# Kernel optimization log

Measured on AMD Instinct MI355X. Metric: run time of the kernel, lower is better.

Reference implementation:

```python
import jax, jax.numpy as jnp
import numpy as np

B, NV, NP, D, K = 8, 2048, 4096, 64, 8  # shapes per batch, vtx/pts counts, feat dim, num_interp
NEG = -1e9


def _unit(x):
    return x / jnp.clip(jnp.linalg.norm(x, axis=-1, keepdims=True), 1e-12)


def _gather(v, idx):
    # v: [B, N, C], idx: [B, Q, K] -> [B, Q, K, C]
    return jax.vmap(lambda a, i: a[i])(v, idx)


def setup_inputs() -> dict:
    key = jax.random.key(0)
    k1, k2, k3, k4, k5 = jax.random.split(key, 5)
    return {
        "vtx": jax.random.normal(k1, (B * NV, 3), jnp.float32),
        "pts": jax.random.normal(k2, (B * NP, 3), jnp.float32),
        "vtx_feature": jax.random.normal(k3, (B * NV, D), jnp.float32),
        "pts_feature": jax.random.normal(k4, (B * NP, D), jnp.float32),
        "vismask_logits": jax.random.normal(k5, (B * NV, 1), jnp.float32),
    }


def reference(vtx, pts, vtx_feature, pts_feature, vismask_logits):
    # --- per-batch min-max normalization of sigmoid(vismask) (serial loop in torch) ---
    vm = jax.nn.sigmoid(vismask_logits).reshape(B, NV, 1)
    vmin = vm.min(axis=1, keepdims=True)
    vmax = vm.max(axis=1, keepdims=True)
    vm = (vm - vmin) / (vmax - vmin)

    vtxb = vtx.reshape(B, NV, 3)
    ptsb = pts.reshape(B, NP, 3)
    vf = vtx_feature.reshape(B, NV, D)
    pf = pts_feature.reshape(B, NP, D)

    # --- cosine KNN: for each vtx, k nearest pts by cosine similarity ---
    sim = jnp.einsum('bnd,bmd->bnm', _unit(vf), _unit(pf))  # [B,NV,NP]
    _, idx = jax.lax.top_k(sim, K)                           # [B,NV,K]

    nbr_pts = _gather(ptsb, idx)                             # [B,NV,K,3]
    nbr_pf = _gather(pf, idx)                                # [B,NV,K,D]
    euclid = nbr_pts - vtxb[:, :, None, :]
    # raw (unnormalized) dot product, weighted by vismask of the query vertex
    fsim = jnp.sum(nbr_pf * vf[:, :, None, :], axis=-1, keepdims=True) * vm[:, :, None, :]
    # scatter_add over assign_index[0] == sum over the K grouped neighbors
    flow_init = jnp.sum(euclid * fsim, axis=2) / jnp.sum(fsim, axis=2)  # [B,NV,3]

    # --- interpolate flow at invisible vertices from visible ones (2nd cosine KNN) ---
    vis = vm >= 0.5                                          # [B,NV,1]
    vfn = _unit(vf)
    sim2 = jnp.einsum('bnd,bmd->bnm', vfn, vfn)              # [B,NV,NV]
    sim2 = jnp.where(vis[:, :, 0][:, None, :], sim2, NEG)    # keys restricted to visible vtx
    _, idx2 = jax.lax.top_k(sim2, K)                         # [B,NV,K]

    nbr_vf = _gather(vf, idx2)                               # [B,NV,K,D]
    nbr_flow = _gather(flow_init, idx2)                      # [B,NV,K,3]
    fsim2 = jnp.sum(nbr_vf * vf[:, :, None, :], axis=-1, keepdims=True)
    invis_flow = jnp.sum(nbr_flow * fsim2, axis=2) / jnp.sum(fsim2, axis=2)

    flow = jnp.where(vis, flow_init, invis_flow)             # flow_init[invis] = invis_flow
    l1_points = jnp.concatenate([flow, vm], axis=-1)         # [B,NV,4]
    return l1_points.reshape(B * NV, 4)
```

## Files before the change

### kernel.cpp

```cpp
#include <hip/hip_runtime.h>
#include <math.h>

#define BB 8
#define NVV 2048
#define NPP 4096
#define DD 64
#define NQ (BB * NVV)
#define QT (NQ / 16)

typedef __attribute__((ext_vector_type(8))) short short8;
typedef __attribute__((ext_vector_type(8))) unsigned short ushort8;
typedef __attribute__((ext_vector_type(4))) float f32x4;

typedef __attribute__((address_space(1))) const unsigned gu32;
typedef __attribute__((address_space(3))) unsigned su32;


__device__ __forceinline__ unsigned short bf16rn(float x) {
  unsigned u = __float_as_uint(x);
  return (unsigned short)((u + 0x7FFFu + ((u >> 16) & 1u)) >> 16);
}
__device__ __forceinline__ float bf2f(unsigned short h) {
  return __uint_as_float(((unsigned)h) << 16);
}

__device__ __forceinline__ void net8(unsigned* a, unsigned v) {
#pragma unroll
  for (int k = 0; k < 7; k++) {
    unsigned r;
    asm("v_med3_u32 %0, %1, %2, %3" : "=v"(r) : "v"(v), "v"(a[k]), "v"(a[k + 1]));
    a[k] = r;
  }
  a[7] = a[7] > v ? a[7] : v;
}

__device__ __forceinline__ unsigned fkey(float s) {
  unsigned u = __float_as_uint(s);
  return ((int)u < 0) ? ~u : (u | 0x80000000u);
}

__global__ __launch_bounds__(256) void k_prep(const float* __restrict__ logits,
                                              const float* __restrict__ vf,
                                              const float* __restrict__ pf,
                                              float* __restrict__ vm,
                                              float* __restrict__ inv_vf_s,
                                              float* __restrict__ inv_pf_s,
                                              unsigned short* __restrict__ vfh,
                                              unsigned short* __restrict__ vfl,
                                              unsigned short* __restrict__ pfh,
                                              unsigned short* __restrict__ pfl,
                                              float* __restrict__ out) {
  int bid = blockIdx.x, t = threadIdx.x;
  if (bid >= 768) {
    int b = bid - 768;
    __shared__ float smn[4], smx[4];
    float vals[8];
    float mn = 1e30f, mx = -1e30f;
#pragma unroll
    for (int i = 0; i < 8; i++) {
      float x = logits[b * NVV + t + i * 256];
      float s = 1.0f / (1.0f + expf(-x));
      vals[i] = s;
      mn = fminf(mn, s);
      mx = fmaxf(mx, s);
    }
    for (int o = 32; o; o >>= 1) {
      mn = fminf(mn, __shfl_xor(mn, o, 64));
      mx = fmaxf(mx, __shfl_xor(mx, o, 64));
    }
    int w = t >> 6;
    if ((t & 63) == 0) { smn[w] = mn; smx[w] = mx; }
    __syncthreads();
    mn = fminf(fminf(smn[0], smn[1]), fminf(smn[2], smn[3]));
    mx = fmaxf(fmaxf(smx[0], smx[1]), fmaxf(smx[2], smx[3]));
    float range = mx - mn;
#pragma unroll
    for (int i = 0; i < 8; i++) {
      float v = (vals[i] - mn) / range;
      int g = b * NVV + t + i * 256;
      vm[g] = v;
      out[g * 4 + 3] = v;
    }
  } else {
    int xcd = bid & 7, kk = bid >> 3;
    int wsel = t >> 6;
    int lane = t & 63, c = lane & 15, quad = (lane >> 4) & 3;
    const float* src;
    unsigned short *dh, *dl;
    float* ginv;
    int tile;
    if (kk < 32) {
      tile = xcd * 128 + kk * 4 + wsel;
      src = vf; dh = vfh; dl = vfl; ginv = inv_vf_s;
    } else {
      tile = xcd * 256 + (kk - 32) * 4 + wsel;
      src = pf; dh = pfh; dl = pfl; ginv = inv_pf_s;
    }
    int row = tile * 16 + c;
    const float* rp = src + (size_t)row * DD + quad * 8;
    float4 a0 = *(const float4*)(rp);
    float4 b0 = *(const float4*)(rp + 4);
    float4 a1 = *(const float4*)(rp + 32);
    float4 b1 = *(const float4*)(rp + 36);
    float xs[16] = {a0.x, a0.y, a0.z, a0.w, b0.x, b0.y, b0.z, b0.w,
                    a1.x, a1.y, a1.z, a1.w, b1.x, b1.y, b1.z, b1.w};
    float ss = 0.f;
#pragma unroll
    for (int j = 0; j < 16; j++) ss = fmaf(xs[j], xs[j], ss);
    ss += __shfl_xor(ss, 16, 64);
    ss += __shfl_xor(ss, 32, 64);
    float inv = 1.0f / fmaxf(sqrtf(ss), 1e-12f);
    if (quad == 0) ginv[row] = 16384.0f * inv;
    ushort8 h, l;
    size_t s0 = (size_t)tile * 128 + lane;
#pragma unroll
    for (int j = 0; j < 8; j++) {
      float xn = xs[j] * inv;
      unsigned short hj = bf16rn(xn);
      h[j] = hj;
      l[j] = bf16rn(xn - bf2f(hj));
    }
    *(ushort8*)(dh + s0 * 8) = h;
    *(ushort8*)(dl + s0 * 8) = l;
#pragma unroll
    for (int j = 0; j < 8; j++) {
      float xn = xs[8 + j] * inv;
      unsigned short hj = bf16rn(xn);
      h[j] = hj;
      l[j] = bf16rn(xn - bf2f(hj));
    }
    *(ushort8*)(dh + (s0 + 64) * 8) = h;
    *(ushort8*)(dl + (s0 + 64) * 8) = l;
  }
}

#define LOADK(d0, d1, d2, d3, KH, KL, tile) do {            \
    size_t bo_ = (size_t)(tile) * 1024 + lane * 8;          \
    d0 = *(const short8*)((KH) + bo_);                      \
    d1 = *(const short8*)((KH) + bo_ + 512);                \
    d2 = *(const short8*)((KL) + bo_);                      \
    d3 = *(const short8*)((KL) + bo_ + 512);                \
  } while (0)

#define MFMA6(c_, h0_, h1_, l0_, l1_) do {                                  \
    c_ = __builtin_amdgcn_mfma_f32_16x16x32_bf16(h0_, qh0, c_, 0, 0, 0);    \
    c_ = __builtin_amdgcn_mfma_f32_16x16x32_bf16(h1_, qh1, c_, 0, 0, 0);    \
    c_ = __builtin_amdgcn_mfma_f32_16x16x32_bf16(h0_, ql0, c_, 0, 0, 0);    \
    c_ = __builtin_amdgcn_mfma_f32_16x16x32_bf16(h1_, ql1, c_, 0, 0, 0);    \
    c_ = __builtin_amdgcn_mfma_f32_16x16x32_bf16(l0_, qh0, c_, 0, 0, 0);    \
    c_ = __builtin_amdgcn_mfma_f32_16x16x32_bf16(l1_, qh1, c_, 0, 0, 0);    \
  } while (0)

#define COMP1(h0_, h1_, l0_, l1_, b16_) do {                                \
    f32x4 c_ = {0.f, 0.f, 0.f, 0.f};                                        \
    MFMA6(c_, h0_, h1_, l0_, l1_);                                          \
    unsigned u0_ = (unsigned)fmaxf(fmaf(c_[0], 520000.0f, 520000.0f), 0.0f);\
    net8(tvA, (u0_ << 12) | (unsigned)((b16_) + 0));                        \
    unsigned u1_ = (unsigned)fmaxf(fmaf(c_[1], 520000.0f, 520000.0f), 0.0f);\
    net8(tvA, (u1_ << 12) | (unsigned)((b16_) + 1));                        \
    unsigned u2_ = (unsigned)fmaxf(fmaf(c_[2], 520000.0f, 520000.0f), 0.0f);\
    net8(tvB, (u2_ << 12) | (unsigned)((b16_) + 2));                        \
    unsigned u3_ = (unsigned)fmaxf(fmaf(c_[3], 520000.0f, 520000.0f), 0.0f);\
    net8(tvB, (u3_ << 12) | (unsigned)((b16_) + 3));                        \
  } while (0)

#define COMP2(h0_, h1_, l0_, l1_, b16_, mp_) do {                           \
    float4 mv_ = *(const float4*)(mp_);                                     \
    f32x4 c_ = {0.f, 0.f, 0.f, 0.f};                                        \
    MFMA6(c_, h0_, h1_, l0_, l1_);                                          \
    unsigned u0_ = (unsigned)fmaxf(fmaf(c_[0], 520000.0f, 520000.0f), 0.0f);\
    unsigned p0_ = (u0_ << 12) | (unsigned)((b16_) + 0);                    \
    net8(tvA, (mv_.x >= 0.5f) ? p0_ : 0u);                                  \
    unsigned u1_ = (unsigned)fmaxf(fmaf(c_[1], 520000.0f, 520000.0f), 0.0f);\
    unsigned p1_ = (u1_ << 12) | (unsigned)((b16_) + 1);                    \
    net8(tvA, (mv_.y >= 0.5f) ? p1_ : 0u);                                  \
    unsigned u2_ = (unsigned)fmaxf(fmaf(c_[2], 520000.0f, 520000.0f), 0.0f);\
    unsigned p2_ = (u2_ << 12) | (unsigned)((b16_) + 2);                    \
    net8(tvB, (mv_.z >= 0.5f) ? p2_ : 0u);                                  \
    unsigned u3_ = (unsigned)fmaxf(fmaf(c_[3], 520000.0f, 520000.0f), 0.0f);\
    unsigned p3_ = (u3_ << 12) | (unsigned)((b16_) + 3);                    \
    net8(tvB, (mv_.w >= 0.5f) ? p3_ : 0u);                                  \
  } while (0)

__global__ __launch_bounds__(256)
void k_knn(const unsigned short* __restrict__ vfh, const unsigned short* __restrict__ vfl,
           const unsigned short* __restrict__ pfh, const unsigned short* __restrict__ pfl,
           const float* __restrict__ vm, unsigned* __restrict__ pc2,
           const float* __restrict__ vf, const float* __restrict__ pf,
           const float* __restrict__ pts, const float* __restrict__ vtx,
           const float* __restrict__ inv_pf_s,
           float* __restrict__ flow_ws, float* __restrict__ out) {
  __shared__ unsigned mg[2][2][16][8];
  __shared__ unsigned cand[16][16];
  __shared__ float rowsLds[4][16][256];
  __shared__ float qrows[16][64];

  int p = blockIdx.x;
  int xcd = p & 7, j = p >> 3;
  int qt_g = xcd * 128 + j;
  int batch = xcd;
  int w = (int)threadIdx.x >> 6;
  int ck = w >> 1, hf = w & 1;
  int lane = threadIdx.x & 63, col = lane & 15, quad = lane >> 4;

  size_t ab = (size_t)qt_g * 1024 + lane * 8;
  short8 qh0 = *(const short8*)(vfh + ab);
  short8 qh1 = *(const short8*)(vfh + ab + 512);
  short8 ql0 = *(const short8*)(vfl + ab);
  short8 ql1 = *(const short8*)(vfl + ab + 512);
  asm volatile("" : "+a"(qh0), "+a"(qh1), "+a"(ql0), "+a"(ql1));

  unsigned tvA[8], tvB[8];

#pragma unroll
  for (int k = 0; k < 8; k++) { tvA[k] = 0u; tvB[k] = 0u; }
  {
    int bt0 = batch * 256 + ck * 128 + hf * 64;
    int tb16 = (ck * 128 + hf * 64) * 16 + quad * 4;
    short8 ah0, ah1, al0, al1, bh0, bh1, bl0, bl1;
    LOADK(ah0, ah1, al0, al1, pfh, pfl, bt0);
#pragma unroll 1
    for (int kt = 0; kt < 62; kt += 2) {
      LOADK(bh0, bh1, bl0, bl1, pfh, pfl, bt0 + kt + 1);
      COMP1(ah0, ah1, al0, al1, tb16 + kt * 16);
      LOADK(ah0, ah1, al0, al1, pfh, pfl, bt0 + kt + 2);
      COMP1(bh0, bh1, bl0, bl1, tb16 + (kt + 1) * 16);
    }
    LOADK(bh0, bh1, bl0, bl1, pfh, pfl, bt0 + 63);
    COMP1(ah0, ah1, al0, al1, tb16 + 62 * 16);
    COMP1(bh0, bh1, bl0, bl1, tb16 + 63 * 16);
  }
#pragma unroll
  for (int k = 0; k < 8; k++) net8(tvA, tvB[k]);
#pragma unroll
  for (int m = 16; m <= 32; m <<= 1) {
    unsigned ov[8];
#pragma unroll
    for (int k = 0; k < 8; k++) ov[k] = (unsigned)__shfl_xor((int)tvA[k], m, 64);
#pragma unroll
    for (int k = 7; k >= 0; k--) net8(tvA, ov[k]);
  }
  if (hf == 1 && quad == 0) {
#pragma unroll
    for (int k = 0; k < 8; k++) mg[0][ck][col][k] = tvA[k];
  }
  __syncthreads();
  if (hf == 0 && quad == 0) {
#pragma unroll
    for (int k = 0; k < 8; k++) net8(tvA, mg[0][ck][col][k]);
#pragma unroll
    for (int k = 0; k < 8; k++)
      cand[col][ck * 8 + k] = tvA[k];
  }
  __syncthreads();

  {
    int tt = (int)threadIdx.x;
    unsigned pkp = cand[tt >> 4][tt & 15];
    const float* gsrc = pf + (size_t)(batch * NPP + (int)(pkp & 0xFFFu)) * DD;
#pragma unroll
    for (int jj = 0; jj < 16; jj++)
      __builtin_amdgcn_global_load_lds((gu32*)(gsrc + jj * 4),
                                       (su32*)&rowsLds[w][jj][0], 16, 0, 0);
    __builtin_amdgcn_global_load_lds(
        (gu32*)(vf + (size_t)qt_g * 1024 + tt * 4),
        (su32*)&qrows[4 * w][0], 16, 0, 0);
  }

#pragma unroll
  for (int k = 0; k < 8; k++) { tvA[k] = 0u; tvB[k] = 0u; }
  {
    const float* mask = vm + batch * NVV;
    int bt0 = batch * 128 + ck * 64 + hf * 32;
    int tbase = ck * 64 + hf * 32;
    int tb16 = tbase * 16 + quad * 4;
    const float* mp0 = mask + tbase * 16 + quad * 4;
    short8 ah0, ah1, al0, al1, bh0, bh1, bl0, bl1;
    LOADK(ah0, ah1, al0, al1, vfh, vfl, bt0);
#pragma unroll 1
    for (int kt = 0; kt < 30; kt += 2) {
      LOADK(bh0, bh1, bl0, bl1, vfh, vfl, bt0 + kt + 1);
      COMP2(ah0, ah1, al0, al1, tb16 + kt * 16, mp0 + kt * 16);
      LOADK(ah0, ah1, al0, al1, vfh, vfl, bt0 + kt + 2);
      COMP2(bh0, bh1, bl0, bl1, tb16 + (kt + 1) * 16, mp0 + (kt + 1) * 16);
    }
    LOADK(bh0, bh1, bl0, bl1, vfh, vfl, bt0 + 31);
    COMP2(ah0, ah1, al0, al1, tb16 + 30 * 16, mp0 + 30 * 16);
    COMP2(bh0, bh1, bl0, bl1, tb16 + 31 * 16, mp0 + 31 * 16);
  }
#pragma unroll
  for (int k = 0; k < 8; k++) net8(tvA, tvB[k]);
#pragma unroll
  for (int m = 16; m <= 32; m <<= 1) {
    unsigned ov[8];
#pragma unroll
    for (int k = 0; k < 8; k++) ov[k] = (unsigned)__shfl_xor((int)tvA[k], m, 64);
#pragma unroll
    for (int k = 7; k >= 0; k--) net8(tvA, ov[k]);
  }
  if (hf == 1 && quad == 0) {
#pragma unroll
    for (int k = 0; k < 8; k++) mg[1][ck][col][k] = tvA[k];
  }
  __syncthreads();
  if (hf == 0 && quad == 0) {
#pragma unroll
    for (int k = 0; k < 8; k++) net8(tvA, mg[1][ck][col][k]);
    int q = qt_g * 16 + col;
#pragma unroll
    for (int k = 0; k < 8; k++)
      pc2[(size_t)(ck * 8 + k) * NQ + q] = tvA[k];
  }
  __syncthreads();

  {
    asm volatile("s_waitcnt vmcnt(0)" ::: "memory");
    int t = (int)threadIdx.x;
    int qloc = t >> 4, c = t & 15;
    int q = qt_g * 16 + qloc;
    int base = lane & 48;

    unsigned pk = cand[qloc][c];
    int id = (int)(pk & 0xFFFu);
    int prow = batch * NPP + id;
    float a0 = 0.f, a1 = 0.f, a2 = 0.f, a3 = 0.f;
#pragma unroll
    for (int jj = 0; jj < 16; jj++) {
      float4 x = *(const float4*)&qrows[qloc][jj * 4];
      float4 y = *(const float4*)&rowsLds[w][jj][lane * 4];
      a0 = fmaf(x.x, y.x, a0);
      a1 = fmaf(x.y, y.y, a1);
      a2 = fmaf(x.z, y.z, a2);
      a3 = fmaf(x.w, y.w, a3);
    }
    float dotv = (a0 + a1) + (a2 + a3);
    float s = dotv * inv_pf_s[prow];
    unsigned kb = fkey(s);

    int rank = 0;
#pragma unroll
    for (int i = 0; i < 16; i++) {
      unsigned ok = (unsigned)__shfl((int)kb, base + i, 64);
      int oid = __shfl(id, base + i, 64);
      rank += (ok > kb || (ok == kb && oid > id)) ? 1 : 0;
    }
    float wgt = (rank < 8) ? dotv : 0.0f;

    float ax = 0.f, ay = 0.f, az = 0.f, den = 0.f;
    if (wgt != 0.0f) {
      ax = (pts[prow * 3 + 0] - vtx[q * 3 + 0]) * wgt;
      ay = (pts[prow * 3 + 1] - vtx[q * 3 + 1]) * wgt;
      az = (pts[prow * 3 + 2] - vtx[q * 3 + 2]) * wgt;
      den = wgt;
    }
#pragma unroll
    for (int m = 1; m <= 8; m <<= 1) {
      ax += __shfl_xor(ax, m, 64);
      ay += __shfl_xor(ay, m, 64);
      az += __shfl_xor(az, m, 64);
      den += __shfl_xor(den, m, 64);
    }
    if (c == 0) {
      float fx = ax / den, fy = ay / den, fz = az / den;
      flow_ws[q * 4 + 0] = fx;
      flow_ws[q * 4 + 1] = fy;
      flow_ws[q * 4 + 2] = fz;
      out[q * 4 + 0] = fx;
      out[q * 4 + 1] = fy;
      out[q * 4 + 2] = fz;
    }
  }
}

__global__ __launch_bounds__(256) void k_merge_final(const unsigned* __restrict__ pc,
                                                     const float* __restrict__ vf,
                                                     const float* __restrict__ vm,
                                                     const float* __restrict__ inv_vf_s,
                                                     const float* __restrict__ flow_ws,
                                                     float* __restrict__ out) {
  __shared__ float qrows[16][64];
  int p = blockIdx.x;
  int xcd = p & 7, jj = p >> 3;
  int lb = xcd * 128 + jj;
  int t = (int)threadIdx.x;
  ((float4*)qrows)[t] = ((const float4*)(vf + (size_t)lb * 16 * DD))[t];
  __syncthreads();

  int q = lb * 16 + (t >> 4), c = t & 15, batch = q >> 11;
  int qloc = t >> 4;
  int lane = t & 63;
  int base = lane & 48;
  bool act = vm[q] < 0.5f;

  unsigned pk = 0u;
  bool valid = false;
  int id = 0;
  float dotv = 0.f, s = 0.f;
  if (act) {
    pk = pc[(size_t)c * NQ + q];
    valid = pk > 0xFFFu;
    id = (int)(pk & 0xFFFu);
    int krow = batch * NVV + id;
    if (valid) {
      const float4* rp = (const float4*)(vf + (size_t)krow * DD);
      float a0 = 0.f, a1 = 0.f, a2 = 0.f, a3 = 0.f;
#pragma unroll
      for (int cc = 0; cc < 16; cc++) {
        float4 x = *(const float4*)&qrows[qloc][cc * 4];
        float4 y = rp[cc];
        a0 = fmaf(x.x, y.x, a0);
        a1 = fmaf(x.y, y.y, a1);
        a2 = fmaf(x.z, y.z, a2);
        a3 = fmaf(x.w, y.w, a3);
      }
      dotv = (a0 + a1) + (a2 + a3);
      s = dotv * inv_vf_s[krow];
    }
  }
  unsigned kb = (act && valid) ? fkey(s) : 0u;

  int rank = 0;
#pragma unroll
  for (int i = 0; i < 16; i++) {
    unsigned ok = (unsigned)__shfl((int)kb, base + i, 64);
    int oid = __shfl(id, base + i, 64);
    rank += (ok > kb || (ok == kb && oid > id)) ? 1 : 0;
  }
  float wgt = (act && valid && rank < 8) ? dotv : 0.0f;

  float ax = 0.f, ay = 0.f, az = 0.f, den = 0.f;
  if (wgt != 0.0f) {
    int krow = batch * NVV + id;
    ax = flow_ws[krow * 4 + 0] * wgt;
    ay = flow_ws[krow * 4 + 1] * wgt;
    az = flow_ws[krow * 4 + 2] * wgt;
    den = wgt;
  }
#pragma unroll
  for (int m = 1; m <= 8; m <<= 1) {
    ax += __shfl_xor(ax, m, 64);
    ay += __shfl_xor(ay, m, 64);
    az += __shfl_xor(az, m, 64);
    den += __shfl_xor(den, m, 64);
  }
  if (act && c == 0) {
    out[q * 4 + 0] = ax / den;
    out[q * 4 + 1] = ay / den;
    out[q * 4 + 2] = az / den;
  }
}

extern "C" void kernel_launch(void* const* d_in, const int* in_sizes, int n_in,
                              void* d_out, int out_size, void* d_ws, size_t ws_size,
                              hipStream_t stream) {
  const float* vtx = (const float*)d_in[0];
  const float* pts = (const float*)d_in[1];
  const float* vf = (const float*)d_in[2];
  const float* pf = (const float*)d_in[3];
  const float* lg = (const float*)d_in[4];
  float* out = (float*)d_out;
  float* ws = (float*)d_ws;

  float* vm = ws;
  float* inv_vf_s = ws + 16384;
  float* inv_pf_s = ws + 32768;
  float* flow = ws + 65536;
  unsigned* pc2 = (unsigned*)(ws + 393216);
  unsigned short* vfh = (unsigned short*)(ws + 655360);
  unsigned short* vfl = (unsigned short*)(ws + 1179648);
  unsigned short* pfh = (unsigned short*)(ws + 1703936);
  unsigned short* pfl = (unsigned short*)(ws + 2752512);

  k_prep<<<768 + BB, 256, 0, stream>>>(lg, vf, pf, vm, inv_vf_s, inv_pf_s,
                                       vfh, vfl, pfh, pfl, out);
  k_knn<<<1024, 256, 0, stream>>>(vfh, vfl, pfh, pfl, vm, pc2,
                                  vf, pf, pts, vtx, inv_pf_s, flow, out);
  k_merge_final<<<NQ * 16 / 256, 256, 0, stream>>>(pc2, vf, vm, inv_vf_s,
                                                   flow, out);
}
```

Baseline: 168.2 us.

## Compute candidate rescoring dot products cooperatively with coalesced loads and shuffle reductions

Both kernels rescored each candidate with one thread reading a whole 64-float row. That used an async global-to-LDS staging of candidate rows in k_knn and strided per-thread row reads in k_merge_final. Now each 16-lane group loads each candidate row together, each lane taking a float4 slice, and the partial dot products are reduced with xor shuffles. This removes the LDS staging buffers and their sync, lowering LDS use and giving coalesced accesses. The cost is 16 shuffle-reduction rounds per query and the loss of the early prefetch, which had overlapped the second KNN phase.

```diff
diff --git a/kernel.cpp b/kernel.cpp
--- a/kernel.cpp
+++ b/kernel.cpp
@@ -11,9 +11,6 @@
 typedef __attribute__((ext_vector_type(8))) short short8;
 typedef __attribute__((ext_vector_type(8))) unsigned short ushort8;
 typedef __attribute__((ext_vector_type(4))) float f32x4;
-
-typedef __attribute__((address_space(1))) const unsigned gu32;
-typedef __attribute__((address_space(3))) unsigned su32;
 
 
 __device__ __forceinline__ unsigned short bf16rn(float x) {
@@ -192,8 +189,6 @@
            float* __restrict__ flow_ws, float* __restrict__ out) {
   __shared__ unsigned mg[2][2][16][8];
   __shared__ unsigned cand[16][16];
-  __shared__ float rowsLds[4][16][256];
-  __shared__ float qrows[16][64];
 
   int p = blockIdx.x;
   int xcd = p & 7, j = p >> 3;
@@ -251,20 +246,6 @@
 #pragma unroll
     for (int k = 0; k < 8; k++)
       cand[col][ck * 8 + k] = tvA[k];
-  }
-  __syncthreads();
-
-  {
-    int tt = (int)threadIdx.x;
-    unsigned pkp = cand[tt >> 4][tt & 15];
-    const float* gsrc = pf + (size_t)(batch * NPP + (int)(pkp & 0xFFFu)) * DD;
-#pragma unroll
-    for (int jj = 0; jj < 16; jj++)
-      __builtin_amdgcn_global_load_lds((gu32*)(gsrc + jj * 4),
-                                       (su32*)&rowsLds[w][jj][0], 16, 0, 0);
-    __builtin_amdgcn_global_load_lds(
-        (gu32*)(vf + (size_t)qt_g * 1024 + tt * 4),
-        (su32*)&qrows[4 * w][0], 16, 0, 0);
   }
 
 #pragma unroll
@@ -314,26 +295,27 @@
   __syncthreads();
 
   {
-    asm volatile("s_waitcnt vmcnt(0)" ::: "memory");
     int t = (int)threadIdx.x;
     int qloc = t >> 4, c = t & 15;
     int q = qt_g * 16 + qloc;
     int base = lane & 48;
 
+    float4 qv = *(const float4*)(vf + (size_t)q * DD + 4 * c);
     unsigned pk = cand[qloc][c];
     int id = (int)(pk & 0xFFFu);
+    float dotv = 0.f;
+#pragma unroll
+    for (int k = 0; k < 16; k++) {
+      int idk = (int)(cand[qloc][k] & 0xFFFu);
+      float4 yv = *(const float4*)(pf + (size_t)(batch * NPP + idk) * DD + 4 * c);
+      float pp = fmaf(qv.x, yv.x, fmaf(qv.y, yv.y, fmaf(qv.z, yv.z, qv.w * yv.w)));
+      pp += __shfl_xor(pp, 1, 64);
+      pp += __shfl_xor(pp, 2, 64);
+      pp += __shfl_xor(pp, 4, 64);
+      pp += __shfl_xor(pp, 8, 64);
+      if (c == k) dotv = pp;
+    }
     int prow = batch * NPP + id;
-    float a0 = 0.f, a1 = 0.f, a2 = 0.f, a3 = 0.f;
-#pragma unroll
-    for (int jj = 0; jj < 16; jj++) {
-      float4 x = *(const float4*)&qrows[qloc][jj * 4];
-      float4 y = *(const float4*)&rowsLds[w][jj][lane * 4];
-      a0 = fmaf(x.x, y.x, a0);
-      a1 = fmaf(x.y, y.y, a1);
-      a2 = fmaf(x.z, y.z, a2);
-      a3 = fmaf(x.w, y.w, a3);
-    }
-    float dotv = (a0 + a1) + (a2 + a3);
     float s = dotv * inv_pf_s[prow];
     unsigned kb = fkey(s);
 
@@ -378,46 +360,43 @@
                                                      const float* __restrict__ inv_vf_s,
                                                      const float* __restrict__ flow_ws,
                                                      float* __restrict__ out) {
-  __shared__ float qrows[16][64];
   int p = blockIdx.x;
   int xcd = p & 7, jj = p >> 3;
   int lb = xcd * 128 + jj;
   int t = (int)threadIdx.x;
-  ((float4*)qrows)[t] = ((const float4*)(vf + (size_t)lb * 16 * DD))[t];
-  __syncthreads();
-
-  int q = lb * 16 + (t >> 4), c = t & 15, batch = q >> 11;
-  int qloc = t >> 4;
+  int qloc = t >> 4, c = t & 15;
+  int q = lb * 16 + qloc, batch = q >> 11;
   int lane = t & 63;
   int base = lane & 48;
   bool act = vm[q] < 0.5f;
 
   unsigned pk = 0u;
-  bool valid = false;
-  int id = 0;
-  float dotv = 0.f, s = 0.f;
+  float4 qv = {0.f, 0.f, 0.f, 0.f};
   if (act) {
     pk = pc[(size_t)c * NQ + q];
-    valid = pk > 0xFFFu;
-    id = (int)(pk & 0xFFFu);
-    int krow = batch * NVV + id;
-    if (valid) {
-      const float4* rp = (const float4*)(vf + (size_t)krow * DD);
-      float a0 = 0.f, a1 = 0.f, a2 = 0.f, a3 = 0.f;
-#pragma unroll
-      for (int cc = 0; cc < 16; cc++) {
-        float4 x = *(const float4*)&qrows[qloc][cc * 4];
-        float4 y = rp[cc];
-        a0 = fmaf(x.x, y.x, a0);
-        a1 = fmaf(x.y, y.y, a1);
-        a2 = fmaf(x.z, y.z, a2);
-        a3 = fmaf(x.w, y.w, a3);
-      }
-      dotv = (a0 + a1) + (a2 + a3);
-      s = dotv * inv_vf_s[krow];
-    }
-  }
-  unsigned kb = (act && valid) ? fkey(s) : 0u;
+    qv = *(const float4*)(vf + (size_t)q * DD + 4 * c);
+  }
+  bool valid = pk > 0xFFFu;
+  int id = (int)(pk & 0xFFFu);
+
+  float dotv = 0.f;
+#pragma unroll
+  for (int k = 0; k < 16; k++) {
+    unsigned pk_k = (unsigned)__shfl((int)pk, base + k, 64);
+    float pp = 0.f;
+    if (act && pk_k > 0xFFFu) {
+      int idk = (int)(pk_k & 0xFFFu);
+      float4 yv = *(const float4*)(vf + (size_t)(batch * NVV + idk) * DD + 4 * c);
+      pp = fmaf(qv.x, yv.x, fmaf(qv.y, yv.y, fmaf(qv.z, yv.z, qv.w * yv.w)));
+    }
+    pp += __shfl_xor(pp, 1, 64);
+    pp += __shfl_xor(pp, 2, 64);
+    pp += __shfl_xor(pp, 4, 64);
+    pp += __shfl_xor(pp, 8, 64);
+    if (c == k) dotv = pp;
+  }
+  unsigned kb = 0u;
+  if (act && valid) kb = fkey(dotv * inv_vf_s[batch * NVV + id]);
 
   int rank = 0;
 #pragma unroll
```

Result: faster. 158.1 us (-6.0%).
